# Kernel tuning notes

Measured on AMD Instinct MI355X. Metric: run time of the kernel, lower is better.

## Reference

```python
import jax, jax.numpy as jnp
import numpy as np

B = 65536
IN1, H, KOUT, GRID, OUT = 784, 128, 64, 10, 10
RICKER_C = 2.0 / (np.sqrt(3.0) * np.pi ** 0.25)


def setup_inputs() -> dict:
    key = jax.random.key(0)
    ks = jax.random.split(key, 8)
    x = jax.random.normal(ks[0], (B, IN1), dtype=jnp.float32)
    w1 = jax.random.normal(ks[1], (H, IN1), dtype=jnp.float32) / np.sqrt(IN1)
    b1 = jnp.zeros((H,), dtype=jnp.float32)
    # wavelet-KAN coefficients: (out, in, gridsize)
    coef = jax.random.normal(ks[2], (KOUT, H, GRID), dtype=jnp.float32) / (
        np.sqrt(H) * np.sqrt(GRID))
    wbias = jnp.zeros((KOUT,), dtype=jnp.float32)
    w2 = jax.random.normal(ks[3], (OUT, KOUT), dtype=jnp.float32) / np.sqrt(KOUT)
    b2 = jnp.zeros((OUT,), dtype=jnp.float32)
    return {"x": x, "w1": w1, "b1": b1, "coef": coef, "wbias": wbias,
            "w2": w2, "b2": b2}


def _ricker(t):
    # Mexican-hat mother wavelet
    return RICKER_C * (1.0 - t * t) * jnp.exp(-0.5 * t * t)


def reference(x, w1, b1, coef, wbias, w2, b2):
    h = x @ w1.T + b1                               # (B, H)
    k = jnp.arange(1, GRID + 1, dtype=h.dtype)      # scales 1..grid
    psi = _ricker(h[:, :, None] * k)                # (B, H, GRID)
    y = jnp.einsum('big,oig->bo', psi, coef) + wbias  # (B, KOUT)
    return y @ w2.T + b2                            # (B, OUT)
```

## Files before the change

### kernel.cpp

```cpp
#include <hip/hip_runtime.h>

typedef short bf16x8 __attribute__((ext_vector_type(8)));
typedef _Float16 f16x8 __attribute__((ext_vector_type(8)));
typedef float f32x4 __attribute__((ext_vector_type(4)));

#define MFMA_BF16(a, b, c) __builtin_amdgcn_mfma_f32_16x16x32_bf16((a), (b), (c), 0, 0, 0)
#define MFMA_F16(a, b, c)  __builtin_amdgcn_mfma_f32_16x16x32_f16((a), (b), (c), 0, 0, 0)

#define STRH 136

__device__ __forceinline__ unsigned int f2bf_rne(float f) {
    unsigned int u = __float_as_uint(f);
    return (u + 0x7FFFu + ((u >> 16) & 1u)) >> 16;
}
__device__ __forceinline__ unsigned int pack_hu(float a, float b) {
    unsigned int ua = (__float_as_uint(a) + 0x8000u) >> 16;
    unsigned int ub = (__float_as_uint(b) + 0x8000u) >> 16;
    return ua | (ub << 16);
}
__device__ __forceinline__ unsigned int pkrtz(float a, float b) {
    return __builtin_bit_cast(unsigned int, __builtin_amdgcn_cvt_pkrtz(a, b));
}

__global__ __launch_bounds__(256) void prep_kernel(
    const float* __restrict__ coef, const float* __restrict__ wbias,
    const float* __restrict__ w2, const float* __restrict__ b2,
    const float* __restrict__ w1, float* __restrict__ ws)
{
    int idx = blockIdx.x * 256 + threadIdx.x;
    if (idx < 20480) {
        int l = (idx >> 3) & 63, j = idx & 7;
        int s = idx >> 9;
        int n = l & 15, q = l >> 4;
        int P = 4 * s + q;
        int g = P >> 4;
        int i = ((P & 15) << 3) + j;
        float v = 0.f;
        if (n < 10) {
            float sum = 0.f;
            const float* cp = coef + i * 10 + g;
            const float* wp = w2 + n * 64;
            #pragma unroll 8
            for (int o = 0; o < 64; ++o)
                sum = fmaf(wp[o], cp[o * 1280], sum);
            v = 0.8673250706f * sum;
        }
        ((unsigned short*)ws)[idx] = (unsigned short)f2bf_rne(v);
    } else if (idx < 20490) {
        int n = idx - 20480;
        float sum = b2[n];
        for (int o = 0; o < 64; ++o)
            sum = fmaf(w2[n * 64 + o], wbias[o], sum);
        ws[10240 + n] = sum;
    } else if (idx >= 20736) {
        int t = idx - 20736;
        if (t < 102400) {
            int n = t / 800, k = t - n * 800;
            _Float16 hv = (_Float16)0.f;
            if (k < 784) hv = (_Float16)w1[n * 784 + k];
            int kt = k >> 5, ko = k & 31;
            int qq = ko >> 3, j = ko & 7;
            int T = n >> 4, ln = qq * 16 + (n & 15);
            int slot = ((kt * 8 + T) * 64 + ln) * 8 + j;
            ((unsigned short*)((char*)ws + 41472))[slot] =
                __builtin_bit_cast(unsigned short, hv);
        }
    }
}

__global__ __launch_bounds__(256, 4) void mnist_fused(
    const float* __restrict__ x, const float* __restrict__ b1,
    const float* __restrict__ ws, float* __restrict__ out)
{
    __shared__ __align__(16) unsigned short h_tile[64 * STRH];
    __shared__ __align__(16) unsigned short c2buf[10240];

    const int tid  = threadIdx.x;
    const int lane = tid & 63;
    const int wv   = tid >> 6;
    const int m    = lane & 15;
    const int q    = lane >> 4;
    const long row0 = (long)blockIdx.x * 64;

    {
        const uint4* src = (const uint4*)ws + tid;
        uint4* dst = (uint4*)c2buf + tid;
        #pragma unroll
        for (int c = 0; c < 5; ++c) dst[c * 256] = src[c * 256];
    }

    const unsigned short* w1f = (const unsigned short*)((const char*)ws + 41472);
    const float* pa = x + (row0 + wv * 16 + m) * 784 + q * 8;

    f32x4 acc[8];
    #pragma unroll
    for (int T = 0; T < 8; ++T) acc[T] = (f32x4){0.f, 0.f, 0.f, 0.f};

    for (int kt = 0; kt < 24; ++kt) {
        float4 a0 = *(const float4*)(pa + kt * 32);
        float4 a1 = *(const float4*)(pa + kt * 32 + 4);
        uint4 b[8];
        #pragma unroll
        for (int T = 0; T < 8; ++T)
            b[T] = *(const uint4*)(w1f + kt * 4096 + T * 512 + lane * 8);
        uint4 ap = make_uint4(pkrtz(a0.x, a0.y), pkrtz(a0.z, a0.w),
                              pkrtz(a1.x, a1.y), pkrtz(a1.z, a1.w));
        f16x8 A = __builtin_bit_cast(f16x8, ap);
        #pragma unroll
        for (int T = 0; T < 8; ++T)
            acc[T] = MFMA_F16(A, __builtin_bit_cast(f16x8, b[T]), acc[T]);
    }
    {
        float4 z4 = make_float4(0.f, 0.f, 0.f, 0.f);
        const float* ps = (q < 2) ? (pa + 768) : pa;
        float4 a0 = (q < 2) ? *(const float4*)(ps)     : z4;
        float4 a1 = (q < 2) ? *(const float4*)(ps + 4) : z4;
        uint4 b[8];
        #pragma unroll
        for (int T = 0; T < 8; ++T)
            b[T] = *(const uint4*)(w1f + 24 * 4096 + T * 512 + lane * 8);
        uint4 ap = make_uint4(pkrtz(a0.x, a0.y), pkrtz(a0.z, a0.w),
                              pkrtz(a1.x, a1.y), pkrtz(a1.z, a1.w));
        f16x8 A = __builtin_bit_cast(f16x8, ap);
        #pragma unroll
        for (int T = 0; T < 8; ++T)
            acc[T] = MFMA_F16(A, __builtin_bit_cast(f16x8, b[T]), acc[T]);
    }

    {
        #pragma unroll
        for (int T = 0; T < 8; ++T) {
            float bias = b1[T * 16 + m];
            #pragma unroll
            for (int r = 0; r < 4; ++r) {
                _Float16 hv = (_Float16)(acc[T][r] + bias);
                h_tile[(wv * 16 + q * 4 + r) * STRH + T * 16 + m] =
                    __builtin_bit_cast(unsigned short, hv);
            }
        }
    }

    f32x4 acc2 = (f32x4){0.f, 0.f, 0.f, 0.f};
    const unsigned short* hrow = h_tile + (wv * 16 + m) * STRH;

    #pragma unroll
    for (int half_ = 0; half_ < 2; ++half_) {
        if (half_ == 1) {
            __syncthreads();
            const uint4* src = (const uint4*)ws + 1280 + tid;
            uint4* dst = (uint4*)c2buf + tid;
            #pragma unroll
            for (int c = 0; c < 5; ++c) dst[c * 256] = src[c * 256];
        }
        __syncthreads();
        #pragma unroll 4
        for (int s2 = 0; s2 < 20; ++s2) {
            int P = (half_ * 20 + s2) * 4 + q;
            float kg = (float)((P >> 4) + 1);
            int i0 = (P & 15) << 3;
            uint4 hraw = *(const uint4*)(hrow + i0);
            f16x8 hh = __builtin_bit_cast(f16x8, hraw);
            unsigned int pk[4];
            #pragma unroll
            for (int e = 0; e < 8; e += 2) {
                float t0 = (float)hh[e] * kg;
                float t1 = (float)hh[e + 1] * kg;
                float z0 = t0 * t0, z1 = t1 * t1;
                float p0 = (1.f - z0) * __expf(-0.5f * z0);
                float p1 = (1.f - z1) * __expf(-0.5f * z1);
                pk[e >> 1] = pack_hu(p0, p1);
            }
            bf16x8 A = __builtin_bit_cast(bf16x8, make_uint4(pk[0], pk[1], pk[2], pk[3]));
            uint4 braw = *(const uint4*)&c2buf[(s2 * 64 + lane) * 8];
            acc2 = MFMA_BF16(A, __builtin_bit_cast(bf16x8, braw), acc2);
        }
    }

    if (m < 10) {
        float bias2 = ws[10240 + m];
        const long rb = row0 + wv * 16 + q * 4;
        #pragma unroll
        for (int r = 0; r < 4; ++r)
            out[(rb + r) * 10 + m] = acc2[r] + bias2;
    }
}

extern "C" void kernel_launch(void* const* d_in, const int* in_sizes, int n_in,
                              void* d_out, int out_size, void* d_ws, size_t ws_size,
                              hipStream_t stream) {
    const float* x     = (const float*)d_in[0];
    const float* w1    = (const float*)d_in[1];
    const float* b1    = (const float*)d_in[2];
    const float* coef  = (const float*)d_in[3];
    const float* wbias = (const float*)d_in[4];
    const float* w2    = (const float*)d_in[5];
    const float* b2    = (const float*)d_in[6];
    float* out = (float*)d_out;
    float* ws  = (float*)d_ws;

    const int Brows = in_sizes[0] / 784;
    prep_kernel<<<481, 256, 0, stream>>>(coef, wbias, w2, b2, w1, ws);
    mnist_fused<<<Brows / 64, 256, 0, stream>>>(x, b1, ws, out);
}
```

Before: 345.4 us.

## Double-buffer W1 tiles in LDS via global_load_lds and switch stage-2 to fp16

Stage 1 now streams each W1 k-tile into a double-buffered LDS region with asynchronous global_load_lds and prefetches the next x chunk, so loads overlap with the MFMAs. The K tail is folded into the main loop by clamping the x pointer; the prep kernel zero-pads W1 past column 784, so those products are zero. Stage 2 stops staging the folded coefficient table in LDS. It reads the table directly from global memory, stores it as fp16 instead of bf16, and uses f16 MFMA with pkrtz packing. The trade is a __syncthreads per k-step, and the fp16 coefficient table shifts rounding behaviour.

```diff
diff --git a/kernel.cpp b/kernel.cpp
--- a/kernel.cpp
+++ b/kernel.cpp
@@ -1,26 +1,18 @@
 #include <hip/hip_runtime.h>
 
-typedef short bf16x8 __attribute__((ext_vector_type(8)));
 typedef _Float16 f16x8 __attribute__((ext_vector_type(8)));
 typedef float f32x4 __attribute__((ext_vector_type(4)));
 
-#define MFMA_BF16(a, b, c) __builtin_amdgcn_mfma_f32_16x16x32_bf16((a), (b), (c), 0, 0, 0)
-#define MFMA_F16(a, b, c)  __builtin_amdgcn_mfma_f32_16x16x32_f16((a), (b), (c), 0, 0, 0)
-
+#define MFMA_F16(a, b, c) __builtin_amdgcn_mfma_f32_16x16x32_f16((a), (b), (c), 0, 0, 0)
 #define STRH 136
 
-__device__ __forceinline__ unsigned int f2bf_rne(float f) {
-    unsigned int u = __float_as_uint(f);
-    return (u + 0x7FFFu + ((u >> 16) & 1u)) >> 16;
-}
-__device__ __forceinline__ unsigned int pack_hu(float a, float b) {
-    unsigned int ua = (__float_as_uint(a) + 0x8000u) >> 16;
-    unsigned int ub = (__float_as_uint(b) + 0x8000u) >> 16;
-    return ua | (ub << 16);
-}
 __device__ __forceinline__ unsigned int pkrtz(float a, float b) {
     return __builtin_bit_cast(unsigned int, __builtin_amdgcn_cvt_pkrtz(a, b));
 }
+
+#define GLDS(g, l) __builtin_amdgcn_global_load_lds(                      \
+    (const __attribute__((address_space(1))) void*)(g),                   \
+    (__attribute__((address_space(3))) void*)(l), 16, 0, 0)
 
 __global__ __launch_bounds__(256) void prep_kernel(
     const float* __restrict__ coef, const float* __restrict__ wbias,
@@ -45,7 +37,8 @@
                 sum = fmaf(wp[o], cp[o * 1280], sum);
             v = 0.8673250706f * sum;
         }
-        ((unsigned short*)ws)[idx] = (unsigned short)f2bf_rne(v);
+        _Float16 hv = (_Float16)v;
+        ((unsigned short*)ws)[idx] = __builtin_bit_cast(unsigned short, hv);
     } else if (idx < 20490) {
         int n = idx - 20480;
         float sum = b2[n];
@@ -72,8 +65,8 @@
     const float* __restrict__ x, const float* __restrict__ b1,
     const float* __restrict__ ws, float* __restrict__ out)
 {
+    __shared__ __align__(16) unsigned short Bbuf[2][4096];
     __shared__ __align__(16) unsigned short h_tile[64 * STRH];
-    __shared__ __align__(16) unsigned short c2buf[10240];
 
     const int tid  = threadIdx.x;
     const int lane = tid & 63;
@@ -82,98 +75,86 @@
     const int q    = lane >> 4;
     const long row0 = (long)blockIdx.x * 64;
 
+    const char* w1f = (const char*)ws + 41472;
+    const float* pa = x + (row0 + wv * 16 + m) * 784 + q * 8;
+
     {
-        const uint4* src = (const uint4*)ws + tid;
-        uint4* dst = (uint4*)c2buf + tid;
-        #pragma unroll
-        for (int c = 0; c < 5; ++c) dst[c * 256] = src[c * 256];
+        const char* g = w1f + wv * 2048 + lane * 16;
+        char* l = (char*)&Bbuf[0][0] + wv * 2048;
+        GLDS(g, l);
+        GLDS(g + 1024, l + 1024);
     }
-
-    const unsigned short* w1f = (const unsigned short*)((const char*)ws + 41472);
-    const float* pa = x + (row0 + wv * 16 + m) * 784 + q * 8;
 
     f32x4 acc[8];
     #pragma unroll
     for (int T = 0; T < 8; ++T) acc[T] = (f32x4){0.f, 0.f, 0.f, 0.f};
 
-    for (int kt = 0; kt < 24; ++kt) {
-        float4 a0 = *(const float4*)(pa + kt * 32);
-        float4 a1 = *(const float4*)(pa + kt * 32 + 4);
-        uint4 b[8];
-        #pragma unroll
-        for (int T = 0; T < 8; ++T)
-            b[T] = *(const uint4*)(w1f + kt * 4096 + T * 512 + lane * 8);
-        uint4 ap = make_uint4(pkrtz(a0.x, a0.y), pkrtz(a0.z, a0.w),
-                              pkrtz(a1.x, a1.y), pkrtz(a1.z, a1.w));
+    float4 xc0 = *(const float4*)pa;
+    float4 xc1 = *(const float4*)(pa + 4);
+
+    for (int kt = 0; kt < 25; ++kt) {
+        __syncthreads();
+        const int cur = kt & 1;
+        if (kt < 24) {
+            const char* g = w1f + (kt + 1) * 8192 + wv * 2048 + lane * 16;
+            char* l = (char*)&Bbuf[cur ^ 1][0] + wv * 2048;
+            GLDS(g, l);
+            GLDS(g + 1024, l + 1024);
+        }
+        float4 xn0 = xc0, xn1 = xc1;
+        if (kt < 24) {
+            int kn = (kt + 1) * 32;
+            const float* p = (kn + q * 8 < 784) ? (pa + kn) : pa;
+            xn0 = *(const float4*)p;
+            xn1 = *(const float4*)(p + 4);
+        }
+        uint4 ap = make_uint4(pkrtz(xc0.x, xc0.y), pkrtz(xc0.z, xc0.w),
+                              pkrtz(xc1.x, xc1.y), pkrtz(xc1.z, xc1.w));
         f16x8 A = __builtin_bit_cast(f16x8, ap);
         #pragma unroll
-        for (int T = 0; T < 8; ++T)
-            acc[T] = MFMA_F16(A, __builtin_bit_cast(f16x8, b[T]), acc[T]);
-    }
-    {
-        float4 z4 = make_float4(0.f, 0.f, 0.f, 0.f);
-        const float* ps = (q < 2) ? (pa + 768) : pa;
-        float4 a0 = (q < 2) ? *(const float4*)(ps)     : z4;
-        float4 a1 = (q < 2) ? *(const float4*)(ps + 4) : z4;
-        uint4 b[8];
-        #pragma unroll
-        for (int T = 0; T < 8; ++T)
-            b[T] = *(const uint4*)(w1f + 24 * 4096 + T * 512 + lane * 8);
-        uint4 ap = make_uint4(pkrtz(a0.x, a0.y), pkrtz(a0.z, a0.w),
-                              pkrtz(a1.x, a1.y), pkrtz(a1.z, a1.w));
-        f16x8 A = __builtin_bit_cast(f16x8, ap);
-        #pragma unroll
-        for (int T = 0; T < 8; ++T)
-            acc[T] = MFMA_F16(A, __builtin_bit_cast(f16x8, b[T]), acc[T]);
+        for (int T = 0; T < 8; ++T) {
+            uint4 braw = *(const uint4*)&Bbuf[cur][T * 512 + lane * 8];
+            acc[T] = MFMA_F16(A, __builtin_bit_cast(f16x8, braw), acc[T]);
+        }
+        xc0 = xn0; xc1 = xn1;
     }
 
-    {
+    #pragma unroll
+    for (int T = 0; T < 8; ++T) {
+        float bias = b1[T * 16 + m];
         #pragma unroll
-        for (int T = 0; T < 8; ++T) {
-            float bias = b1[T * 16 + m];
-            #pragma unroll
-            for (int r = 0; r < 4; ++r) {
-                _Float16 hv = (_Float16)(acc[T][r] + bias);
-                h_tile[(wv * 16 + q * 4 + r) * STRH + T * 16 + m] =
-                    __builtin_bit_cast(unsigned short, hv);
-            }
+        for (int r = 0; r < 4; ++r) {
+            _Float16 hv = (_Float16)(acc[T][r] + bias);
+            h_tile[(wv * 16 + q * 4 + r) * STRH + T * 16 + m] =
+                __builtin_bit_cast(unsigned short, hv);
         }
     }
+    __syncthreads();
 
     f32x4 acc2 = (f32x4){0.f, 0.f, 0.f, 0.f};
     const unsigned short* hrow = h_tile + (wv * 16 + m) * STRH;
+    const uint4* c2g = (const uint4*)ws;
 
-    #pragma unroll
-    for (int half_ = 0; half_ < 2; ++half_) {
-        if (half_ == 1) {
-            __syncthreads();
-            const uint4* src = (const uint4*)ws + 1280 + tid;
-            uint4* dst = (uint4*)c2buf + tid;
-            #pragma unroll
-            for (int c = 0; c < 5; ++c) dst[c * 256] = src[c * 256];
+    #pragma unroll 8
+    for (int s2 = 0; s2 < 40; ++s2) {
+        int P = s2 * 4 + q;
+        float kg = (float)((P >> 4) + 1);
+        int i0 = (P & 15) << 3;
+        uint4 hraw = *(const uint4*)(hrow + i0);
+        f16x8 hh = __builtin_bit_cast(f16x8, hraw);
+        unsigned int pk[4];
+        #pragma unroll
+        for (int e = 0; e < 8; e += 2) {
+            float t0 = (float)hh[e] * kg;
+            float t1 = (float)hh[e + 1] * kg;
+            float z0 = t0 * t0, z1 = t1 * t1;
+            float p0 = (1.f - z0) * __expf(-0.5f * z0);
+            float p1 = (1.f - z1) * __expf(-0.5f * z1);
+            pk[e >> 1] = pkrtz(p0, p1);
         }
-        __syncthreads();
-        #pragma unroll 4
-        for (int s2 = 0; s2 < 20; ++s2) {
-            int P = (half_ * 20 + s2) * 4 + q;
-            float kg = (float)((P >> 4) + 1);
-            int i0 = (P & 15) << 3;
-            uint4 hraw = *(const uint4*)(hrow + i0);
-            f16x8 hh = __builtin_bit_cast(f16x8, hraw);
-            unsigned int pk[4];
-            #pragma unroll
-            for (int e = 0; e < 8; e += 2) {
-                float t0 = (float)hh[e] * kg;
-                float t1 = (float)hh[e + 1] * kg;
-                float z0 = t0 * t0, z1 = t1 * t1;
-                float p0 = (1.f - z0) * __expf(-0.5f * z0);
-                float p1 = (1.f - z1) * __expf(-0.5f * z1);
-                pk[e >> 1] = pack_hu(p0, p1);
-            }
-            bf16x8 A = __builtin_bit_cast(bf16x8, make_uint4(pk[0], pk[1], pk[2], pk[3]));
-            uint4 braw = *(const uint4*)&c2buf[(s2 * 64 + lane) * 8];
-            acc2 = MFMA_BF16(A, __builtin_bit_cast(bf16x8, braw), acc2);
-        }
+        uint4 braw = c2g[s2 * 64 + lane];
+        acc2 = MFMA_F16(__builtin_bit_cast(f16x8, make_uint4(pk[0], pk[1], pk[2], pk[3])),
+                        __builtin_bit_cast(f16x8, braw), acc2);
     }
 
     if (m < 10) {
```

Measured after the change: 325.4 us. 5.8% less time.
